# Performance work log

Hardware: AMD Instinct MI355X
Metric: run time of the kernel (lower is better)

The kernel has to match this reference:

```python
import jax, jax.numpy as jnp
import numpy as np

N_EMBD = 512
N_HEADS = 8
D_HEAD = N_EMBD // N_HEADS


def setup_inputs() -> dict:
    key = jax.random.key(0)
    k1, k2, k3, k4, k5 = jax.random.split(key, 5)
    B, T = 4, 2048
    scale = 1.0 / np.sqrt(N_EMBD)
    return {
        "x": jax.random.normal(k1, (B, T, N_EMBD), dtype=jnp.float32),
        # fused QKV projection: Linear(n_embd, 3*n_embd)
        "W_attn": jax.random.normal(k2, (N_EMBD, 3 * N_EMBD), dtype=jnp.float32) * scale,
        "b_attn": jax.random.normal(k3, (3 * N_EMBD,), dtype=jnp.float32) * 0.01,
        # output projection: Linear(n_embd, n_embd)
        "W_out": jax.random.normal(k4, (N_EMBD, N_EMBD), dtype=jnp.float32) * scale,
        "b_out": jax.random.normal(k5, (N_EMBD,), dtype=jnp.float32) * 0.01,
    }


def reference(x, W_attn, b_attn, W_out, b_out):
    B, T, C = x.shape
    # fused QKV projection then split
    qkv = x @ W_attn + b_attn  # [B, T, 3C]
    q, k, v = jnp.split(qkv, 3, axis=-1)
    # [B, T, C] -> [B, H, T, Dh]
    def heads(t):
        return t.reshape(B, T, N_HEADS, D_HEAD).transpose(0, 2, 1, 3)
    q, k, v = heads(q), heads(k), heads(v)
    # scaled dot-product attention (non-causal, no mask; dropout off in eval)
    scores = jnp.einsum("bhqd,bhkd->bhqk", q, k) / jnp.sqrt(jnp.float32(D_HEAD))
    attn = jax.nn.softmax(scores, axis=-1)
    y = jnp.einsum("bhqk,bhkd->bhqd", attn, v)  # [B, H, T, Dh]
    y = y.transpose(0, 2, 1, 3).reshape(B, T, C)
    # output projection (resid dropout off in eval)
    return y @ W_out + b_out
```

## Files before the change

### kernel.cpp

```cpp
#include <hip/hip_runtime.h>

typedef __attribute__((ext_vector_type(8))) short bf16x8;
typedef __attribute__((ext_vector_type(4))) float f32x4;
typedef unsigned short u16;
typedef unsigned int u32;

#define MFMA16(A, B, C) __builtin_amdgcn_mfma_f32_16x16x32_bf16((A), (B), (C), 0, 0, 0)

#if __has_builtin(__builtin_amdgcn_exp2f)
#define EXP2(x) __builtin_amdgcn_exp2f(x)
#else
#define EXP2(x) exp2f(x)
#endif

typedef __attribute__((address_space(3))) unsigned int lds_u32;
typedef const __attribute__((address_space(1))) unsigned int glb_u32;

__device__ __forceinline__ u16 f2bf(float f) {
  union { float f; unsigned u; } x; x.f = f;
  unsigned r = (x.u + 0x7fffu + ((x.u >> 16) & 1u)) >> 16;
  return (u16)r;
}
__device__ __forceinline__ float bf2f(u16 h) {
  union { float f; unsigned u; } x; x.u = ((unsigned)h) << 16;
  return x.f;
}

__device__ __forceinline__ void stage_sw64(const u16* src, u16* lds, int tid) {
#pragma unroll
  for (int i = 0; i < 2; i++) {
    int vv = tid + i * 256;
    int row = vv >> 3, c = vv & 7;
    const u16* gp = src + (size_t)row * 64 + (size_t)(c ^ (row & 7)) * 8;
    __builtin_amdgcn_global_load_lds((glb_u32*)gp,
        (lds_u32*)(lds + (size_t)(i * 256 + (tid & 192)) * 8), 16, 0, 0);
  }
}


__global__ __launch_bounds__(256) void cast_x_kernel(const float* __restrict__ x,
                                                     u16* __restrict__ xb, int n4) {
  int i = blockIdx.x * 256 + threadIdx.x;
  if (i >= n4) return;
  float4 v = ((const float4*)x)[i];
  ushort4 o;
  o.x = f2bf(v.x); o.y = f2bf(v.y); o.z = f2bf(v.z); o.w = f2bf(v.w);
  ((ushort4*)xb)[i] = o;
}

__global__ __launch_bounds__(256) void trans_wa_kernel(const float* __restrict__ W,
                                                       u16* __restrict__ wta) {
  __shared__ u16 T[64][72];
  const int n0 = blockIdx.x * 64;
  const int k0 = blockIdx.y * 64;
  const int tid = threadIdx.x;
  const int r = tid >> 4, c4 = (tid & 15) * 4;
#pragma unroll
  for (int i = 0; i < 4; i++) {
    int row = r + i * 16;
    float4 v = *(const float4*)&W[(size_t)(k0 + row) * 1536 + n0 + c4];
    T[c4 + 0][row] = f2bf(v.x);
    T[c4 + 1][row] = f2bf(v.y);
    T[c4 + 2][row] = f2bf(v.z);
    T[c4 + 3][row] = f2bf(v.w);
  }
  __syncthreads();
  const int row = tid >> 2, c16 = (tid & 3) * 16;
  *(uint4*)&wta[(size_t)(n0 + row) * 512 + k0 + c16]     = *(uint4*)&T[row][c16];
  *(uint4*)&wta[(size_t)(n0 + row) * 512 + k0 + c16 + 8] = *(uint4*)&T[row][c16 + 8];
}

__global__ __launch_bounds__(256) void trans_wo_kernel(const float* __restrict__ W,
                                                       u16* __restrict__ whi,
                                                       u16* __restrict__ wlo) {
  __shared__ u16 Th[64][72];
  __shared__ u16 Tl[64][72];
  const int n0 = blockIdx.x * 64;
  const int k0 = blockIdx.y * 64;
  const int tid = threadIdx.x;
  const int r = tid >> 4, c4 = (tid & 15) * 4;
#pragma unroll
  for (int i = 0; i < 4; i++) {
    int row = r + i * 16;
    float4 v = *(const float4*)&W[(size_t)(k0 + row) * 512 + n0 + c4];
    float vv[4] = {v.x, v.y, v.z, v.w};
#pragma unroll
    for (int jj = 0; jj < 4; jj++) {
      u16 hi = f2bf(vv[jj]);
      Th[c4 + jj][row] = hi;
      Tl[c4 + jj][row] = f2bf(vv[jj] - bf2f(hi));
    }
  }
  __syncthreads();
  const int row = tid >> 2, c16 = (tid & 3) * 16;
  *(uint4*)&whi[(size_t)(n0 + row) * 512 + k0 + c16]     = *(uint4*)&Th[row][c16];
  *(uint4*)&whi[(size_t)(n0 + row) * 512 + k0 + c16 + 8] = *(uint4*)&Th[row][c16 + 8];
  *(uint4*)&wlo[(size_t)(n0 + row) * 512 + k0 + c16]     = *(uint4*)&Tl[row][c16];
  *(uint4*)&wlo[(size_t)(n0 + row) * 512 + k0 + c16 + 8] = *(uint4*)&Tl[row][c16 + 8];
}

__global__ __launch_bounds__(256) void gemm_qkv(const u16* __restrict__ xb,
                                                const u16* __restrict__ wta,
                                                const float* __restrict__ b_attn,
                                                u16* __restrict__ q,
                                                u16* __restrict__ kk,
                                                u16* __restrict__ v) {
  __shared__ u16 A_lds[2][64 * 72];
  __shared__ u16 B_lds[2][64 * 72];
  const int bid = blockIdx.x;
  const int xcd = bid & 7, rr = bid >> 3;
  const int m0 = (xcd * 16 + (rr & 15)) * 64;
  const int n0 = (rr >> 4) * 64;
  const int tid  = threadIdx.x;
  const int lane = tid & 63, w = tid >> 6;
  const int wm = w >> 1, wn = w & 1;
  const int quad = lane >> 4, l15 = lane & 15;

  f32x4 acc[2][2] = {};

  uint4 ra[2], rb[2];
#pragma unroll
  for (int i = 0; i < 2; i++) {
    int vv = tid + i * 256;
    int row = vv >> 3, cv = (vv & 7) * 8;
    ra[i] = *(const uint4*)(xb  + (size_t)(m0 + row) * 512 + cv);
    rb[i] = *(const uint4*)(wta + (size_t)(n0 + row) * 512 + cv);
  }

  for (int kt = 0; kt < 8; kt++) {
    u16* Ab = A_lds[kt & 1];
    u16* Bb = B_lds[kt & 1];
#pragma unroll
    for (int i = 0; i < 2; i++) {
      int vv = tid + i * 256;
      int row = vv >> 3, cv = (vv & 7) * 8;
      *(uint4*)&Ab[row * 72 + cv] = ra[i];
      *(uint4*)&Bb[row * 72 + cv] = rb[i];
    }
    __syncthreads();
    if (kt < 7) {
      int k0 = (kt + 1) * 64;
#pragma unroll
      for (int i = 0; i < 2; i++) {
        int vv = tid + i * 256;
        int row = vv >> 3, cv = (vv & 7) * 8;
        ra[i] = *(const uint4*)(xb  + (size_t)(m0 + row) * 512 + k0 + cv);
        rb[i] = *(const uint4*)(wta + (size_t)(n0 + row) * 512 + k0 + cv);
      }
    }
#pragma unroll
    for (int ks = 0; ks < 2; ks++) {
      bf16x8 af[2], bf[2];
#pragma unroll
      for (int ri = 0; ri < 2; ri++)
        af[ri] = *(const bf16x8*)&Ab[(wm * 32 + ri * 16 + l15) * 72 + ks * 32 + quad * 8];
#pragma unroll
      for (int ci = 0; ci < 2; ci++)
        bf[ci] = *(const bf16x8*)&Bb[(wn * 32 + ci * 16 + l15) * 72 + ks * 32 + quad * 8];
#pragma unroll
      for (int ri = 0; ri < 2; ri++)
#pragma unroll
        for (int ci = 0; ci < 2; ci++)
          acc[ri][ci] = MFMA16(af[ri], bf[ci], acc[ri][ci]);
    }
  }

  const float QS = 0.18033688011112043f;
#pragma unroll
  for (int ri = 0; ri < 2; ri++) {
#pragma unroll
    for (int ci = 0; ci < 2; ci++) {
      int n = n0 + wn * 32 + ci * 16 + l15;
      float bias = b_attn[n];
      int chunk = n >> 9;
      int c = n & 511;
      int h = c >> 6, d = c & 63;
      int m_base = m0 + wm * 32 + ri * 16 + quad * 4;
      int b = m_base >> 11, t0 = m_base & 2047;
      int bh = b * 8 + h;
      if (chunk == 0) {
#pragma unroll
        for (int r = 0; r < 4; r++)
          q[(size_t)(bh * 2048 + t0 + r) * 64 + d] = f2bf((acc[ri][ci][r] + bias) * QS);
      } else if (chunk == 1) {
#pragma unroll
        for (int r = 0; r < 4; r++)
          kk[(size_t)(bh * 2048 + t0 + r) * 64 + d] = f2bf(acc[ri][ci][r] + bias);
      } else {
        int it = t0 >> 7, ks2 = (t0 >> 5) & 3, qd = (t0 >> 3) & 3, jj = t0 & 7;
        ushort4 pk;
        pk.x = f2bf(acc[ri][ci][0] + bias);
        pk.y = f2bf(acc[ri][ci][1] + bias);
        pk.z = f2bf(acc[ri][ci][2] + bias);
        pk.w = f2bf(acc[ri][ci][3] + bias);
        size_t idx = ((((size_t)bh * 16 + it) * 4 + ks2) * 64 + d) * 32 + qd * 8 + jj;
        *(ushort4*)&v[idx] = pk;
      }
    }
  }
}

__global__ __launch_bounds__(256, 4) void flash_attn(const u16* __restrict__ q,
                                                     const u16* __restrict__ k,
                                                     const u16* __restrict__ vt,
                                                     u16* __restrict__ yb) {
  __shared__ u16 K_lds[2][64 * 64];
  __shared__ u16 P_lds[4 * 2 * 16 * 72];

  const int flat = blockIdx.y * 16 + blockIdx.x;
  const int bh = (flat & 7) * 4 + ((flat >> 3) & 3);
  const int qt = flat >> 5;

  const int tid  = threadIdx.x;
  const int lane = tid & 63, w = tid >> 6;
  const int quad = lane >> 4, l15 = lane & 15;
  const int sw0 = ((quad)     ^ (l15 & 7)) * 8;
  const int sw1 = ((quad + 4) ^ (l15 & 7)) * 8;

  const u16* qp = q  + (size_t)bh * 131072;
  const u16* kp = k  + (size_t)bh * 131072;
  const u16* vp = vt + (size_t)bh * 131072;

  bf16x8 qf[2];
#pragma unroll
  for (int ks = 0; ks < 2; ks++)
    qf[ks] = *(const bf16x8*)(qp + (size_t)(qt * 64 + w * 16 + l15) * 64 + ks * 32 + quad * 8);

  f32x4 l_acc = {};
  f32x4 o[4] = {};

  bf16x8 ones;
  {
    short one = (short)0x3F80;
    ones = (bf16x8){one, one, one, one, one, one, one, one};
  }

  u16* Pw = &P_lds[w * 2 * 16 * 72];

#define S_PHASE(KB, PB)                                                        \
  do {                                                                         \
    _Pragma("unroll")                                                          \
    for (int jt = 0; jt < 4; jt++) {                                           \
      bf16x8 kf0 = *(const bf16x8*)&(KB)[(jt * 16 + l15) * 64 + sw0];          \
      bf16x8 kf1 = *(const bf16x8*)&(KB)[(jt * 16 + l15) * 64 + sw1];          \
      f32x4 s = {0.f, 0.f, 0.f, 0.f};                                          \
      s = MFMA16(kf0, qf[0], s);                                               \
      s = MFMA16(kf1, qf[1], s);                                               \
      u32 pb[4];                                                               \
      _Pragma("unroll")                                                        \
      for (int r = 0; r < 4; r++) pb[r] = __float_as_uint(EXP2(s[r]));         \
      uint2 pk;                                                                \
      pk.x = __builtin_amdgcn_perm(pb[1], pb[0], 0x07060302u);                 \
      pk.y = __builtin_amdgcn_perm(pb[3], pb[2], 0x07060302u);                 \
      *(uint2*)&(PB)[l15 * 72 + jt * 16 + quad * 4] = pk;                      \
    }                                                                          \
  } while (0)

#define PV_PHASE(VIT, PB)                                                      \
  do {                                                                         \
    bf16x8 vf[2][4];                                                           \
    _Pragma("unroll")                                                          \
    for (int dt = 0; dt < 4; dt++)                                             \
      vf[0][dt] = *(const bf16x8*)((VIT) + (dt * 16 + l15) * 32 + quad * 8);   \
    _Pragma("unroll")                                                          \
    for (int dt = 0; dt < 4; dt++)                                             \
      vf[1][dt] = *(const bf16x8*)((VIT) + 2048 + (dt * 16 + l15) * 32 + quad * 8); \
    __builtin_amdgcn_s_setprio(1);                                             \
    _Pragma("unroll")                                                          \
    for (int ks = 0; ks < 2; ks++) {                                           \
      bf16x8 pf = *(const bf16x8*)&(PB)[l15 * 72 + ks * 32 + quad * 8];        \
      l_acc = MFMA16(pf, ones, l_acc);                                         \
      _Pragma("unroll")                                                        \
      for (int dt = 0; dt < 4; dt++)                                           \
        o[dt] = MFMA16(pf, vf[ks][dt], o[dt]);                                 \
    }                                                                          \
    __builtin_amdgcn_s_setprio(0);                                             \
  } while (0)

  stage_sw64(kp, K_lds[0], tid);
  stage_sw64(kp + 4096, K_lds[1], tid);
  __syncthreads();
  S_PHASE(K_lds[0], Pw);

  for (int it = 0; it < 31; it++) {
    __syncthreads();
    if (it < 30) stage_sw64(kp + (size_t)(it + 2) * 4096, K_lds[it & 1], tid);
    u16* Pc = Pw + (it & 1) * 16 * 72;
    u16* Pn = Pw + ((it + 1) & 1) * 16 * 72;
    S_PHASE(K_lds[(it + 1) & 1], Pn);
    PV_PHASE(vp + (it) * 4096, Pc);
  }
  PV_PHASE(vp + 31 * 4096, Pw + (31 & 1) * 16 * 72);

#undef S_PHASE
#undef PV_PHASE

  const int b = bh >> 3, h = bh & 7;
  u32* Tw = (u32*)Pw;
#pragma unroll
  for (int r = 0; r < 4; r++) {
    float inv = 1.f / l_acc[r];
#pragma unroll
    for (int dt = 0; dt < 4; dt++) {
      float val = o[dt][r] * inv;
      u16 hi = f2bf(val);
      u16 lo = f2bf(val - bf2f(hi));
      Tw[(quad * 4 + r) * 68 + dt * 16 + l15] = (u32)hi | ((u32)lo << 16);
    }
  }
  {
    int t = qt * 64 + w * 16 + l15;
    size_t rowb = (size_t)(b * 2048 + t) * 512 + h * 64 + quad * 16;
    uint4 g0 = *(uint4*)&Tw[l15 * 68 + quad * 16 + 0];
    uint4 g1 = *(uint4*)&Tw[l15 * 68 + quad * 16 + 4];
    uint4 g2 = *(uint4*)&Tw[l15 * 68 + quad * 16 + 8];
    uint4 g3 = *(uint4*)&Tw[l15 * 68 + quad * 16 + 12];
    uint4 hi4, lo4;
    hi4.x = __builtin_amdgcn_perm(g0.y, g0.x, 0x05040100u);
    hi4.y = __builtin_amdgcn_perm(g0.w, g0.z, 0x05040100u);
    hi4.z = __builtin_amdgcn_perm(g1.y, g1.x, 0x05040100u);
    hi4.w = __builtin_amdgcn_perm(g1.w, g1.z, 0x05040100u);
    lo4.x = __builtin_amdgcn_perm(g0.y, g0.x, 0x07060302u);
    lo4.y = __builtin_amdgcn_perm(g0.w, g0.z, 0x07060302u);
    lo4.z = __builtin_amdgcn_perm(g1.y, g1.x, 0x07060302u);
    lo4.w = __builtin_amdgcn_perm(g1.w, g1.z, 0x07060302u);
    *(uint4*)&yb[rowb] = hi4;
    *(uint4*)&yb[(size_t)4 * 2048 * 512 + rowb] = lo4;
    hi4.x = __builtin_amdgcn_perm(g2.y, g2.x, 0x05040100u);
    hi4.y = __builtin_amdgcn_perm(g2.w, g2.z, 0x05040100u);
    hi4.z = __builtin_amdgcn_perm(g3.y, g3.x, 0x05040100u);
    hi4.w = __builtin_amdgcn_perm(g3.w, g3.z, 0x05040100u);
    lo4.x = __builtin_amdgcn_perm(g2.y, g2.x, 0x07060302u);
    lo4.y = __builtin_amdgcn_perm(g2.w, g2.z, 0x07060302u);
    lo4.z = __builtin_amdgcn_perm(g3.y, g3.x, 0x07060302u);
    lo4.w = __builtin_amdgcn_perm(g3.w, g3.z, 0x07060302u);
    *(uint4*)&yb[rowb + 8] = hi4;
    *(uint4*)&yb[(size_t)4 * 2048 * 512 + rowb + 8] = lo4;
  }
}

__global__ __launch_bounds__(256) void gemm_out(const u16* __restrict__ yhi,
                                                const u16* __restrict__ ylo,
                                                const u16* __restrict__ whi,
                                                const u16* __restrict__ wlo,
                                                const float* __restrict__ b_out,
                                                float* __restrict__ out) {
  __shared__ u16 Ah[64 * 72];
  __shared__ u16 Al[64 * 72];
  __shared__ u16 Bh[64 * 72];
  __shared__ u16 Bl[64 * 72];
  const int bid = blockIdx.x;
  const int xcd = bid & 7, rr = bid >> 3;
  const int m0 = (xcd * 16 + (rr & 15)) * 64;
  const int n0 = (rr >> 4) * 64;
  const int tid  = threadIdx.x;
  const int lane = tid & 63, w = tid >> 6;
  const int wm = w >> 1, wn = w & 1;
  const int quad = lane >> 4, l15 = lane & 15;

  f32x4 acc[2][2] = {};

  for (int k0 = 0; k0 < 512; k0 += 64) {
#pragma unroll
    for (int i = 0; i < 2; i++) {
      int vv = tid + i * 256;
      int row = vv >> 3;
      int cv  = (vv & 7) * 8;
      *(uint4*)&Ah[row * 72 + cv] = *(const uint4*)(yhi + (size_t)(m0 + row) * 512 + k0 + cv);
      *(uint4*)&Al[row * 72 + cv] = *(const uint4*)(ylo + (size_t)(m0 + row) * 512 + k0 + cv);
      *(uint4*)&Bh[row * 72 + cv] = *(const uint4*)(whi + (size_t)(n0 + row) * 512 + k0 + cv);
      *(uint4*)&Bl[row * 72 + cv] = *(const uint4*)(wlo + (size_t)(n0 + row) * 512 + k0 + cv);
    }
    __syncthreads();
#pragma unroll
    for (int ks = 0; ks < 2; ks++) {
      bf16x8 afh[2], afl[2], bfh[2], bfl[2];
#pragma unroll
      for (int ri = 0; ri < 2; ri++) {
        afh[ri] = *(const bf16x8*)&Ah[(wm * 32 + ri * 16 + l15) * 72 + ks * 32 + quad * 8];
        afl[ri] = *(const bf16x8*)&Al[(wm * 32 + ri * 16 + l15) * 72 + ks * 32 + quad * 8];
      }
#pragma unroll
      for (int ci = 0; ci < 2; ci++) {
        bfh[ci] = *(const bf16x8*)&Bh[(wn * 32 + ci * 16 + l15) * 72 + ks * 32 + quad * 8];
        bfl[ci] = *(const bf16x8*)&Bl[(wn * 32 + ci * 16 + l15) * 72 + ks * 32 + quad * 8];
      }
#pragma unroll
      for (int ri = 0; ri < 2; ri++)
#pragma unroll
        for (int ci = 0; ci < 2; ci++) {
          acc[ri][ci] = MFMA16(afh[ri], bfh[ci], acc[ri][ci]);
          acc[ri][ci] = MFMA16(afh[ri], bfl[ci], acc[ri][ci]);
          acc[ri][ci] = MFMA16(afl[ri], bfh[ci], acc[ri][ci]);
        }
    }
    __syncthreads();
  }

#pragma unroll
  for (int ri = 0; ri < 2; ri++) {
#pragma unroll
    for (int ci = 0; ci < 2; ci++) {
      int n = n0 + wn * 32 + ci * 16 + l15;
      float bias = b_out[n];
#pragma unroll
      for (int r = 0; r < 4; r++) {
        int m = m0 + wm * 32 + ri * 16 + quad * 4 + r;
        out[(size_t)m * 512 + n] = acc[ri][ci][r] + bias;
      }
    }
  }
}

extern "C" void kernel_launch(void* const* d_in, const int* in_sizes, int n_in,
                              void* d_out, int out_size, void* d_ws, size_t ws_size,
                              hipStream_t stream) {
  const float* x      = (const float*)d_in[0];
  const float* W_attn = (const float*)d_in[1];
  const float* b_attn = (const float*)d_in[2];
  const float* W_out  = (const float*)d_in[3];
  const float* b_out  = (const float*)d_in[4];
  float* out = (float*)d_out;

  char* ws = (char*)d_ws;
  u16* xb   = (u16*)(ws + 0);
  u16* wta  = (u16*)(ws + 8388608);
  u16* wtoh = (u16*)(ws + 9961472);
  u16* wtol = (u16*)(ws + 10485760);
  u16* qb   = (u16*)(ws + 11010048);
  u16* kb   = (u16*)(ws + 19398656);
  u16* vtb  = (u16*)(ws + 27787264);
  u16* yhi  = (u16*)(ws + 36175872);

  cast_x_kernel<<<4096, 256, 0, stream>>>(x, xb, 4 * 2048 * 512 / 4);
  trans_wa_kernel<<<dim3(24, 8), 256, 0, stream>>>(W_attn, wta);
  trans_wo_kernel<<<dim3(8, 8), 256, 0, stream>>>(W_out, wtoh, wtol);
  gemm_qkv<<<3072, 256, 0, stream>>>(xb, wta, b_attn, qb, kb, vtb);
  flash_attn<<<dim3(16, 64), 256, 0, stream>>>(qb, kb, vtb, yhi);
  gemm_out<<<1024, 256, 0, stream>>>(yhi, yhi + (size_t)4 * 2048 * 512, wtoh, wtol, b_out, out);
}
```

Baseline: 196.3 us.

## Enlarge GEMM tiles and stage operands via direct global-to-LDS swizzled loads

```diff
diff --git a/kernel.cpp b/kernel.cpp
--- a/kernel.cpp
+++ b/kernel.cpp
@@ -32,6 +32,18 @@
     int vv = tid + i * 256;
     int row = vv >> 3, c = vv & 7;
     const u16* gp = src + (size_t)row * 64 + (size_t)(c ^ (row & 7)) * 8;
+    __builtin_amdgcn_global_load_lds((glb_u32*)gp,
+        (lds_u32*)(lds + (size_t)(i * 256 + (tid & 192)) * 8), 16, 0, 0);
+  }
+}
+
+template <int ROWS>
+__device__ __forceinline__ void stage_ld512(const u16* src, u16* lds, int tid) {
+#pragma unroll
+  for (int i = 0; i < ROWS / 32; i++) {
+    int vv = tid + i * 256;
+    int row = vv >> 3, c = vv & 7;
+    const u16* gp = src + (size_t)row * 512 + (size_t)(c ^ (row & 7)) * 8;
     __builtin_amdgcn_global_load_lds((glb_u32*)gp,
         (lds_u32*)(lds + (size_t)(i * 256 + (tid & 192)) * 8), 16, 0, 0);
   }
@@ -105,77 +117,55 @@
                                                 u16* __restrict__ q,
                                                 u16* __restrict__ kk,
                                                 u16* __restrict__ v) {
-  __shared__ u16 A_lds[2][64 * 72];
-  __shared__ u16 B_lds[2][64 * 72];
+  __shared__ u16 A_lds[128 * 64];
+  __shared__ u16 B_lds[128 * 64];
   const int bid = blockIdx.x;
   const int xcd = bid & 7, rr = bid >> 3;
-  const int m0 = (xcd * 16 + (rr & 15)) * 64;
-  const int n0 = (rr >> 4) * 64;
+  const int m0 = (xcd * 8 + (rr & 7)) * 128;
+  const int n0 = (rr >> 3) * 128;
   const int tid  = threadIdx.x;
   const int lane = tid & 63, w = tid >> 6;
   const int wm = w >> 1, wn = w & 1;
   const int quad = lane >> 4, l15 = lane & 15;
-
-  f32x4 acc[2][2] = {};
-
-  uint4 ra[2], rb[2];
-#pragma unroll
-  for (int i = 0; i < 2; i++) {
-    int vv = tid + i * 256;
-    int row = vv >> 3, cv = (vv & 7) * 8;
-    ra[i] = *(const uint4*)(xb  + (size_t)(m0 + row) * 512 + cv);
-    rb[i] = *(const uint4*)(wta + (size_t)(n0 + row) * 512 + cv);
-  }
+  const int sw0 = ((quad)     ^ (l15 & 7)) * 8;
+  const int sw1 = ((quad + 4) ^ (l15 & 7)) * 8;
+
+  f32x4 acc[4][4] = {};
 
   for (int kt = 0; kt < 8; kt++) {
-    u16* Ab = A_lds[kt & 1];
-    u16* Bb = B_lds[kt & 1];
-#pragma unroll
-    for (int i = 0; i < 2; i++) {
-      int vv = tid + i * 256;
-      int row = vv >> 3, cv = (vv & 7) * 8;
-      *(uint4*)&Ab[row * 72 + cv] = ra[i];
-      *(uint4*)&Bb[row * 72 + cv] = rb[i];
-    }
+    stage_ld512<128>(xb  + (size_t)m0 * 512 + kt * 64, A_lds, tid);
+    stage_ld512<128>(wta + (size_t)n0 * 512 + kt * 64, B_lds, tid);
     __syncthreads();
-    if (kt < 7) {
-      int k0 = (kt + 1) * 64;
-#pragma unroll
-      for (int i = 0; i < 2; i++) {
-        int vv = tid + i * 256;
-        int row = vv >> 3, cv = (vv & 7) * 8;
-        ra[i] = *(const uint4*)(xb  + (size_t)(m0 + row) * 512 + k0 + cv);
-        rb[i] = *(const uint4*)(wta + (size_t)(n0 + row) * 512 + k0 + cv);
-      }
-    }
 #pragma unroll
     for (int ks = 0; ks < 2; ks++) {
-      bf16x8 af[2], bf[2];
-#pragma unroll
-      for (int ri = 0; ri < 2; ri++)
-        af[ri] = *(const bf16x8*)&Ab[(wm * 32 + ri * 16 + l15) * 72 + ks * 32 + quad * 8];
-#pragma unroll
-      for (int ci = 0; ci < 2; ci++)
-        bf[ci] = *(const bf16x8*)&Bb[(wn * 32 + ci * 16 + l15) * 72 + ks * 32 + quad * 8];
-#pragma unroll
-      for (int ri = 0; ri < 2; ri++)
-#pragma unroll
-        for (int ci = 0; ci < 2; ci++)
+      const int sw = ks ? sw1 : sw0;
+      bf16x8 af[4], bf[4];
+#pragma unroll
+      for (int ri = 0; ri < 4; ri++)
+        af[ri] = *(const bf16x8*)&A_lds[(wm * 64 + ri * 16 + l15) * 64 + sw];
+#pragma unroll
+      for (int ci = 0; ci < 4; ci++)
+        bf[ci] = *(const bf16x8*)&B_lds[(wn * 64 + ci * 16 + l15) * 64 + sw];
+#pragma unroll
+      for (int ri = 0; ri < 4; ri++)
+#pragma unroll
+        for (int ci = 0; ci < 4; ci++)
           acc[ri][ci] = MFMA16(af[ri], bf[ci], acc[ri][ci]);
     }
+    __syncthreads();
   }
 
   const float QS = 0.18033688011112043f;
 #pragma unroll
-  for (int ri = 0; ri < 2; ri++) {
-#pragma unroll
-    for (int ci = 0; ci < 2; ci++) {
-      int n = n0 + wn * 32 + ci * 16 + l15;
+  for (int ri = 0; ri < 4; ri++) {
+#pragma unroll
+    for (int ci = 0; ci < 4; ci++) {
+      int n = n0 + wn * 64 + ci * 16 + l15;
       float bias = b_attn[n];
       int chunk = n >> 9;
       int c = n & 511;
       int h = c >> 6, d = c & 63;
-      int m_base = m0 + wm * 32 + ri * 16 + quad * 4;
+      int m_base = m0 + wm * 64 + ri * 16 + quad * 4;
       int b = m_base >> 11, t0 = m_base & 2047;
       int bh = b * 8 + h;
       if (chunk == 0) {
@@ -345,48 +335,46 @@
                                                 const u16* __restrict__ wlo,
                                                 const float* __restrict__ b_out,
                                                 float* __restrict__ out) {
-  __shared__ u16 Ah[64 * 72];
-  __shared__ u16 Al[64 * 72];
-  __shared__ u16 Bh[64 * 72];
-  __shared__ u16 Bl[64 * 72];
+  __shared__ u16 Ah[128 * 64];
+  __shared__ u16 Al[128 * 64];
+  __shared__ u16 Bh[64 * 64];
+  __shared__ u16 Bl[64 * 64];
   const int bid = blockIdx.x;
   const int xcd = bid & 7, rr = bid >> 3;
-  const int m0 = (xcd * 16 + (rr & 15)) * 64;
-  const int n0 = (rr >> 4) * 64;
+  const int m0 = (xcd * 8 + (rr & 7)) * 128;
+  const int n0 = (rr >> 3) * 64;
   const int tid  = threadIdx.x;
   const int lane = tid & 63, w = tid >> 6;
   const int wm = w >> 1, wn = w & 1;
   const int quad = lane >> 4, l15 = lane & 15;
-
-  f32x4 acc[2][2] = {};
-
-  for (int k0 = 0; k0 < 512; k0 += 64) {
-#pragma unroll
-    for (int i = 0; i < 2; i++) {
-      int vv = tid + i * 256;
-      int row = vv >> 3;
-      int cv  = (vv & 7) * 8;
-      *(uint4*)&Ah[row * 72 + cv] = *(const uint4*)(yhi + (size_t)(m0 + row) * 512 + k0 + cv);
-      *(uint4*)&Al[row * 72 + cv] = *(const uint4*)(ylo + (size_t)(m0 + row) * 512 + k0 + cv);
-      *(uint4*)&Bh[row * 72 + cv] = *(const uint4*)(whi + (size_t)(n0 + row) * 512 + k0 + cv);
-      *(uint4*)&Bl[row * 72 + cv] = *(const uint4*)(wlo + (size_t)(n0 + row) * 512 + k0 + cv);
-    }
+  const int sw0 = ((quad)     ^ (l15 & 7)) * 8;
+  const int sw1 = ((quad + 4) ^ (l15 & 7)) * 8;
+
+  f32x4 acc[4][2] = {};
+
+  for (int kt = 0; kt < 8; kt++) {
+    const int k0 = kt * 64;
+    stage_ld512<128>(yhi + (size_t)m0 * 512 + k0, Ah, tid);
+    stage_ld512<128>(ylo + (size_t)m0 * 512 + k0, Al, tid);
+    stage_ld512<64>(whi + (size_t)n0 * 512 + k0, Bh, tid);
+    stage_ld512<64>(wlo + (size_t)n0 * 512 + k0, Bl, tid);
     __syncthreads();
 #pragma unroll
     for (int ks = 0; ks < 2; ks++) {
-      bf16x8 afh[2], afl[2], bfh[2], bfl[2];
-#pragma unroll
-      for (int ri = 0; ri < 2; ri++) {
-        afh[ri] = *(const bf16x8*)&Ah[(wm * 32 + ri * 16 + l15) * 72 + ks * 32 + quad * 8];
-        afl[ri] = *(const bf16x8*)&Al[(wm * 32 + ri * 16 + l15) * 72 + ks * 32 + quad * 8];
+      const int sw = ks ? sw1 : sw0;
+      bf16x8 afh[4], afl[4], bfh[2], bfl[2];
+#pragma unroll
+      for (int ri = 0; ri < 4; ri++) {
+        afh[ri] = *(const bf16x8*)&Ah[(wm * 64 + ri * 16 + l15) * 64 + sw];
+        afl[ri] = *(const bf16x8*)&Al[(wm * 64 + ri * 16 + l15) * 64 + sw];
       }
 #pragma unroll
       for (int ci = 0; ci < 2; ci++) {
-        bfh[ci] = *(const bf16x8*)&Bh[(wn * 32 + ci * 16 + l15) * 72 + ks * 32 + quad * 8];
-        bfl[ci] = *(const bf16x8*)&Bl[(wn * 32 + ci * 16 + l15) * 72 + ks * 32 + quad * 8];
+        bfh[ci] = *(const bf16x8*)&Bh[(wn * 32 + ci * 16 + l15) * 64 + sw];
+        bfl[ci] = *(const bf16x8*)&Bl[(wn * 32 + ci * 16 + l15) * 64 + sw];
       }
 #pragma unroll
-      for (int ri = 0; ri < 2; ri++)
+      for (int ri = 0; ri < 4; ri++)
 #pragma unroll
         for (int ci = 0; ci < 2; ci++) {
           acc[ri][ci] = MFMA16(afh[ri], bfh[ci], acc[ri][ci]);
@@ -398,14 +386,14 @@
   }
 
 #pragma unroll
-  for (int ri = 0; ri < 2; ri++) {
+  for (int ri = 0; ri < 4; ri++) {
 #pragma unroll
     for (int ci = 0; ci < 2; ci++) {
       int n = n0 + wn * 32 + ci * 16 + l15;
       float bias = b_out[n];
 #pragma unroll
       for (int r = 0; r < 4; r++) {
-        int m = m0 + wm * 32 + ri * 16 + quad * 4 + r;
+        int m = m0 + wm * 64 + ri * 16 + quad * 4 + r;
         out[(size_t)m * 512 + n] = acc[ri][ci][r] + bias;
       }
     }
@@ -435,7 +423,7 @@
   cast_x_kernel<<<4096, 256, 0, stream>>>(x, xb, 4 * 2048 * 512 / 4);
   trans_wa_kernel<<<dim3(24, 8), 256, 0, stream>>>(W_attn, wta);
   trans_wo_kernel<<<dim3(8, 8), 256, 0, stream>>>(W_out, wtoh, wtol);
-  gemm_qkv<<<3072, 256, 0, stream>>>(xb, wta, b_attn, qb, kb, vtb);
+  gemm_qkv<<<768, 256, 0, stream>>>(xb, wta, b_attn, qb, kb, vtb);
   flash_attn<<<dim3(16, 64), 256, 0, stream>>>(qb, kb, vtb, yhi);
-  gemm_out<<<1024, 256, 0, stream>>>(yhi, yhi + (size_t)4 * 2048 * 512, wtoh, wtol, b_out, out);
-}
+  gemm_out<<<512, 256, 0, stream>>>(yhi, yhi + (size_t)4 * 2048 * 512, wtoh, wtol, b_out, out);
+}
```

Measured after the change: 195.4 us. Within noise of the previous version (-0.4%).
